# Optimization experiments

Hardware: AMD Instinct MI355X
Metric: run time of the kernel (lower is better)

## Reference

```python
import jax, jax.numpy as jnp
import numpy as np

B, S, H, D = 8, 1024, 8, 64      # batch, seq_len, num_heads, num_hidden
DM = H * D                        # input model dim = 512
DK = 64.0                         # d_k scale
EPS = 1e-3                        # keras GroupNormalization default epsilon


def setup_inputs() -> dict:
    key = jax.random.key(0)
    ks = jax.random.split(key, 12)
    sc = 1.0 / np.sqrt(DM)
    return {
        "query":  jax.random.normal(ks[0], (B, S, DM), jnp.float32),
        "key":    jax.random.normal(ks[1], (B, S, DM), jnp.float32),
        "values": jax.random.normal(ks[2], (B, S, DM), jnp.float32),
        "Wq": jax.random.normal(ks[3], (DM, 3 * H * D), jnp.float32) * sc,
        "bq": jnp.zeros((3 * H * D,), jnp.float32),
        "Wk": jax.random.normal(ks[4], (DM, 2 * H * D), jnp.float32) * sc,
        "bk": jnp.zeros((2 * H * D,), jnp.float32),
        "Wv": jax.random.normal(ks[5], (DM, H * D), jnp.float32) * sc,
        "bv": jnp.zeros((H * D,), jnp.float32),
        "gamma": jnp.ones((D,), jnp.float32),
        "beta": jnp.zeros((D,), jnp.float32),
        "lam": jax.random.uniform(ks[6], (1,), jnp.float32),          # trainable lambda
        "lambda_init": jax.random.uniform(ks[7], (1,), jnp.float32),  # frozen lambda_init
    }


def reference(query, key, values, Wq, bq, Wk, bk, Wv, bv, gamma, beta, lam, lambda_init):
    # projections -> (B, H, S, *)
    q = (query @ Wq + bq).reshape(B, S, H, 3 * D).transpose(0, 2, 1, 3)
    k = (key @ Wk + bk).reshape(B, S, H, 2 * D).transpose(0, 2, 1, 3)
    v = (values @ Wv + bv).reshape(B, S, H, D).transpose(0, 2, 1, 3)

    q1, q2, gate = jnp.split(q, 3, axis=-1)      # each (B,H,S,D)
    k1, k2 = k[..., :D], k[..., D:]

    inv = 1.0 / jnp.sqrt(jnp.float32(DK))
    s1 = jnp.einsum("bhqd,bhkd->bhqk", q1, k1) * inv
    s2 = jnp.einsum("bhqd,bhkd->bhqk", q2, k2) * inv

    # differential attention: dual softmax combined with learned lambda
    attn = jax.nn.softmax(s1, axis=-1) - lam[0] * jax.nn.softmax(s2, axis=-1)
    out = jnp.einsum("bhqk,bhkd->bhqd", attn, v)      # (B,H,S,D)
    out = out.transpose(0, 2, 1, 3)                    # (B,S,H,D)

    # keras GroupNormalization(groups=H, axis=-1) on channels D:
    # reshape channel dim into (groups, D//H), reduce over all non-batch,
    # non-group axes: (S, H, D//H)
    g = out.reshape(B, S, H, H, D // H)
    mean = jnp.mean(g, axis=(1, 2, 4), keepdims=True)
    var = jnp.var(g, axis=(1, 2, 4), keepdims=True)
    g = (g - mean) * jax.lax.rsqrt(var + EPS)
    out = g.reshape(B, S, H, D) * gamma + beta

    out = out * (1.0 - lambda_init[0])
    out = out * jax.nn.sigmoid(gate.transpose(0, 2, 1, 3))
    return out.reshape(B, S, H * D)
```

## Files before the change

### kernel.cpp

```cpp
#include <hip/hip_runtime.h>
#include <cstdint>
#include <cstddef>

#define B_ 8
#define S_ 1024
#define H_ 8
#define D_ 64
#define DM_ 512

typedef __bf16 bf16x8 __attribute__((ext_vector_type(8)));
typedef float floatx4 __attribute__((ext_vector_type(4)));
typedef unsigned short ushort8 __attribute__((ext_vector_type(8)));
typedef unsigned short ushort4v __attribute__((ext_vector_type(4)));

union Frag { ushort8 us; bf16x8 bf; };
union FragU { uint32_t u[4]; bf16x8 bf; };

#define MFMA(a, b, c) __builtin_amdgcn_mfma_f32_16x16x32_bf16((a), (b), (c), 0, 0, 0)

__device__ __forceinline__ unsigned short f2bf(float f) {
  unsigned int u = __float_as_uint(f);
  unsigned int r = (u + 0x7fffu + ((u >> 16) & 1u)) >> 16;
  return (unsigned short)r;
}

__device__ __forceinline__ void gload16(const void* g, void* l) {
  __builtin_amdgcn_global_load_lds(
      (const __attribute__((address_space(1))) unsigned int*)g,
      (__attribute__((address_space(3))) unsigned int*)l, 16, 0, 0);
}

__global__ __launch_bounds__(256) void prep_kernel(
    const float* __restrict__ q, const float* __restrict__ k,
    const float* __restrict__ v, unsigned short* __restrict__ abf,
    const float* __restrict__ Wq, const float* __restrict__ Wk,
    const float* __restrict__ Wv, unsigned short* __restrict__ wt)
{
  __shared__ unsigned short sT[64][72];
  const int tid = threadIdx.x;
  if (blockIdx.x < 12288) {
    size_t i4 = ((size_t)blockIdx.x * 256 + tid) * 4;
    const size_t SEG = (size_t)4 << 20;
    const float* src = (i4 < SEG) ? (q + i4)
                     : (i4 < 2 * SEG) ? (k + (i4 - SEG))
                                      : (v + (i4 - 2 * SEG));
    floatx4 f = *(const floatx4*)src;
    ushort4v o;
    o[0] = f2bf(f[0]); o[1] = f2bf(f[1]); o[2] = f2bf(f[2]); o[3] = f2bf(f[3]);
    *(ushort4v*)(abf + i4) = o;
    return;
  }
  const int bid = blockIdx.x - 12288;
  const int k0 = (bid & 7) * 64;
  const int n0 = (bid >> 3) * 64;
  const float* src; int ncols, nb;
  if (n0 < 1536)      { src = Wq; ncols = 1536; nb = n0; }
  else if (n0 < 2560) { src = Wk; ncols = 1024; nb = n0 - 1536; }
  else                { src = Wv; ncols = 512;  nb = n0 - 2560; }

  const int kr0 = tid >> 4, nc4 = (tid & 15) * 4;
  #pragma unroll
  for (int i = 0; i < 4; i++) {
    int kr = kr0 + i * 16;
    floatx4 f = *(const floatx4*)(src + (size_t)(k0 + kr) * ncols + nb + nc4);
    sT[nc4 + 0][kr] = f2bf(f[0]);
    sT[nc4 + 1][kr] = f2bf(f[1]);
    sT[nc4 + 2][kr] = f2bf(f[2]);
    sT[nc4 + 3][kr] = f2bf(f[3]);
  }
  __syncthreads();
  const int nr0 = tid >> 3, kc8 = (tid & 7) * 8;
  #pragma unroll
  for (int i = 0; i < 2; i++) {
    int nr = nr0 + i * 32;
    *(ushort8*)(wt + (size_t)(n0 + nr) * 512 + k0 + kc8) = *(const ushort8*)&sT[nr][kc8];
  }
}

__global__ __launch_bounds__(256) void gemm_kernel(
    const unsigned short* __restrict__ abf, const unsigned short* __restrict__ wt,
    const float* __restrict__ bq, const float* __restrict__ bk,
    const float* __restrict__ bv,
    unsigned short* __restrict__ q1, unsigned short* __restrict__ q2,
    float* __restrict__ gate, unsigned short* __restrict__ k1,
    unsigned short* __restrict__ k2, unsigned short* __restrict__ vT)
{
  const int tid  = threadIdx.x;
  const int wave = tid >> 6;
  const int lane = tid & 63;
  const int l16  = lane & 15;
  const int quad = lane >> 4;
  const int mt = blockIdx.x;
  const int nt = blockIdx.y;
  const int wm = wave & 1, wn = wave >> 1;

  const unsigned short* Asrc =
      abf + (nt < 12 ? 0 : nt < 20 ? ((size_t)4 << 20) : ((size_t)8 << 20));

  __shared__ unsigned short sMem[2 * 128 * 64];
  unsigned short* sA = sMem;
  unsigned short* sB = sMem + 128 * 64;

  floatx4 acc[4][4];
  #pragma unroll
  for (int i = 0; i < 4; i++)
    #pragma unroll
    for (int j = 0; j < 4; j++)
      #pragma unroll
      for (int r = 0; r < 4; r++) acc[i][j][r] = 0.0f;

  const int lrow   = lane >> 3;
  const int lchunk = lane & 7;
  const int gchunk = lchunk ^ lrow;
  const int rkey   = l16 & 7;

  for (int kt = 0; kt < 8; kt++) {
    #pragma unroll
    for (int j = 0; j < 4; j++) {
      int r8 = (wave * 4 + j) * 8;
      gload16(Asrc + (size_t)(mt * 128 + r8 + lrow) * 512 + kt * 64 + gchunk * 8,
              &sA[(wave * 4 + j) * 512]);
      gload16(wt + (size_t)(nt * 128 + r8 + lrow) * 512 + kt * 64 + gchunk * 8,
              &sB[(wave * 4 + j) * 512]);
    }
    __syncthreads();
    #pragma unroll
    for (int c = 0; c < 2; c++) {
      Frag af[4], bf[4];
      #pragma unroll
      for (int mi = 0; mi < 4; mi++)
        af[mi].us = *(const ushort8*)&sA[(wm * 64 + mi * 16 + l16) * 64 +
                                         (((c * 4 + quad) ^ rkey) << 3)];
      #pragma unroll
      for (int ni = 0; ni < 4; ni++)
        bf[ni].us = *(const ushort8*)&sB[(wn * 64 + ni * 16 + l16) * 64 +
                                         (((c * 4 + quad) ^ rkey) << 3)];
      #pragma unroll
      for (int mi = 0; mi < 4; mi++)
        #pragma unroll
        for (int ni = 0; ni < 4; ni++)
          acc[mi][ni] = MFMA(af[mi].bf, bf[ni].bf, acc[mi][ni]);
    }
    __syncthreads();
  }

  const int gm0 = mt * 128 + wm * 64;
  const int bb  = gm0 >> 10;
  const int s0  = gm0 & 1023;
  const int nseg = nt * 2 + wn;
  unsigned short* sC = sMem + wave * 4096;

  int h, sel = 0; bool isV = false;
  const float* bias_arr; int nb0;
  unsigned short* dstb = nullptr;
  if (nseg < 24)      { h = nseg / 3; sel = nseg % 3; bias_arr = bq; nb0 = nseg * 64;
                        dstb = (sel == 0) ? q1 : (sel == 1) ? q2 : nullptr; }
  else if (nseg < 40) { int t = nseg - 24; h = t >> 1; sel = t & 1;
                        bias_arr = bk; nb0 = t * 64; dstb = sel ? k2 : k1; }
  else                { h = nseg - 40; isV = true; bias_arr = bv; nb0 = (nseg - 40) * 64; }

  if (dstb != nullptr || isV) {
    #pragma unroll
    for (int ni = 0; ni < 4; ni++) {
      float bv_ = bias_arr[nb0 + ni * 16 + l16];
      #pragma unroll
      for (int mi = 0; mi < 4; mi++)
        #pragma unroll
        for (int r = 0; r < 4; r++) {
          float val = acc[mi][ni][r] + bv_;
          int ml = mi * 16 + quad * 4 + r;
          int nl = ni * 16 + l16;
          if (!isV) {
            int ch = (nl >> 3) ^ (ml & 7);
            sC[ml * 64 + (ch << 3) + (nl & 7)] = f2bf(val);
          } else {
            int ch = (ml >> 3) ^ (nl & 7);
            sC[nl * 64 + (ch << 3) + (ml & 7)] = f2bf(val);
          }
        }
    }
    const int rr = lane >> 3, cc = lane & 7;
    if (!isV) {
      unsigned short* base = dstb + ((size_t)(bb * H_ + h) * S_ + s0) * D_;
      #pragma unroll
      for (int j = 0; j < 8; j++) {
        int row = j * 8 + rr;
        int logc = cc ^ (row & 7);
        ushort8 valv = *(const ushort8*)&sC[row * 64 + cc * 8];
        *(ushort8*)(base + (size_t)row * D_ + logc * 8) = valv;
      }
    } else {
      unsigned short* base = vT + ((size_t)(bb * H_ + h) * D_) * S_ + s0;
      #pragma unroll
      for (int j = 0; j < 8; j++) {
        int drow = j * 8 + rr;
        int logc = cc ^ (drow & 7);
        ushort8 valv = *(const ushort8*)&sC[drow * 64 + cc * 8];
        *(ushort8*)(base + (size_t)drow * S_ + logc * 8) = valv;
      }
    }
  } else {
    #pragma unroll
    for (int ni = 0; ni < 4; ni++) {
      float bv_ = bias_arr[nb0 + ni * 16 + l16];
      #pragma unroll
      for (int mi = 0; mi < 4; mi++)
        #pragma unroll
        for (int r = 0; r < 4; r++) {
          int s = s0 + mi * 16 + quad * 4 + r;
          int d = ni * 16 + l16;
          gate[((size_t)(bb * H_ + h) * S_ + s) * D_ + d] = acc[mi][ni][r] + bv_;
        }
    }
  }
}

__global__ __launch_bounds__(256, 4) void attn_kernel(
    const unsigned short* __restrict__ q1, const unsigned short* __restrict__ q2,
    const unsigned short* __restrict__ k1, const unsigned short* __restrict__ k2,
    const unsigned short* __restrict__ vT, const float* __restrict__ lamp,
    float* __restrict__ O)
{
  const int tid  = threadIdx.x;
  const int wave = tid >> 6;
  const int lane = tid & 63;
  const int l16  = lane & 15;
  const int quad = lane >> 4;
  const int bh = blockIdx.x & 63;
  const int qt = blockIdx.x >> 6;

  __shared__ unsigned short sMem[3 * 4096];
  unsigned short* sK1 = sMem;
  unsigned short* sK2 = sMem + 4096;
  unsigned short* sVt = sMem + 8192;

  const int q0 = qt * 64;
  const size_t qoff = ((size_t)bh * S_ + q0 + wave * 16 + l16) * D_;
  Frag qf1[2], qf2[2];
  #pragma unroll
  for (int c = 0; c < 2; c++) {
    qf1[c].us = *(const ushort8*)(q1 + qoff + c * 32 + quad * 8);
    qf2[c].us = *(const ushort8*)(q2 + qoff + c * 32 + quad * 8);
  }

  floatx4 o1t[4], o2t[4];
  float l1 = 0.f, l2 = 0.f;
  #pragma unroll
  for (int i = 0; i < 4; i++)
    #pragma unroll
    for (int j = 0; j < 4; j++) { o1t[i][j] = 0.f; o2t[i][j] = 0.f; }

  const unsigned short* kb1 = k1 + (size_t)bh * S_ * D_;
  const unsigned short* kb2 = k2 + (size_t)bh * S_ * D_;
  const unsigned short* vb  = vT + (size_t)bh * D_ * S_;

  const int srow = lane >> 3;
  const int sgch = (lane & 7) ^ srow;
  const int rkey = l16 & 7;

  for (int kt = 0; kt < 16; kt++) {
    #pragma unroll
    for (int i = 0; i < 2; i++) {
      int r0 = wave * 16 + i * 8;
      gload16(kb1 + (size_t)(kt * 64 + r0 + srow) * 64 + sgch * 8, &sK1[r0 * 64]);
      gload16(kb2 + (size_t)(kt * 64 + r0 + srow) * 64 + sgch * 8, &sK2[r0 * 64]);
      gload16(vb  + (size_t)(r0 + srow) * S_ + kt * 64 + sgch * 8, &sVt[r0 * 64]);
    }
    __syncthreads();

    floatx4 s1[4], s2[4];
    #pragma unroll
    for (int nt = 0; nt < 4; nt++)
      #pragma unroll
      for (int j = 0; j < 4; j++) { s1[nt][j] = 0.f; s2[nt][j] = 0.f; }
    #pragma unroll
    for (int c = 0; c < 2; c++)
      #pragma unroll
      for (int nt = 0; nt < 4; nt++) {
        Frag kf1; kf1.us = *(const ushort8*)&sK1[(nt * 16 + l16) * 64 +
                                                 (((c * 4 + quad) ^ rkey) << 3)];
        s1[nt] = MFMA(kf1.bf, qf1[c].bf, s1[nt]);
        Frag kf2; kf2.us = *(const ushort8*)&sK2[(nt * 16 + l16) * 64 +
                                                 (((c * 4 + quad) ^ rkey) << 3)];
        s2[nt] = MFMA(kf2.bf, qf2[c].bf, s2[nt]);
      }

    uint32_t pk1[4][2], pk2[4][2];
    #pragma unroll
    for (int nt = 0; nt < 4; nt++)
      #pragma unroll
      for (int h = 0; h < 2; h++) {
        float a1 = __expf(s1[nt][2 * h]     * 0.125f);
        float b1v = __expf(s1[nt][2 * h + 1] * 0.125f);
        l1 += a1 + b1v;
        pk1[nt][h] = (uint32_t)f2bf(a1) | ((uint32_t)f2bf(b1v) << 16);
        float a2 = __expf(s2[nt][2 * h]     * 0.125f);
        float b2v = __expf(s2[nt][2 * h + 1] * 0.125f);
        l2 += a2 + b2v;
        pk2[nt][h] = (uint32_t)f2bf(a2) | ((uint32_t)f2bf(b2v) << 16);
      }

    #pragma unroll
    for (int c = 0; c < 2; c++) {
      FragU b1, b2;
      #pragma unroll
      for (int p = 0; p < 4; p++) {
        int src = l16 + ((((quad << 1) + (p >> 1)) & 3) << 4);
        int h = p & 1;
        int lo1 = __shfl((int)pk1[c * 2][h],     src, 64);
        int hi1 = __shfl((int)pk1[c * 2 + 1][h], src, 64);
        b1.u[p] = (quad & 2) ? (uint32_t)hi1 : (uint32_t)lo1;
        int lo2 = __shfl((int)pk2[c * 2][h],     src, 64);
        int hi2 = __shfl((int)pk2[c * 2 + 1][h], src, 64);
        b2.u[p] = (quad & 2) ? (uint32_t)hi2 : (uint32_t)lo2;
      }
      #pragma unroll
      for (int dt = 0; dt < 4; dt++) {
        Frag vf; vf.us = *(const ushort8*)&sVt[(dt * 16 + l16) * 64 +
                                               (((c * 4 + quad) ^ rkey) << 3)];
        o1t[dt] = MFMA(vf.bf, b1.bf, o1t[dt]);
        o2t[dt] = MFMA(vf.bf, b2.bf, o2t[dt]);
      }
    }
    __syncthreads();
  }

  l1 += __shfl_xor(l1, 16, 64); l1 += __shfl_xor(l1, 32, 64);
  l2 += __shfl_xor(l2, 16, 64); l2 += __shfl_xor(l2, 32, 64);

  const float lam = lamp[0];
  const float i1 = 1.0f / l1;
  const float i2 = lam / l2;

  float* fO = (float*)sMem;
  #pragma unroll
  for (int dt = 0; dt < 4; dt++)
    #pragma unroll
    for (int r = 0; r < 4; r++) {
      int d = dt * 16 + quad * 4 + r;
      fO[d * 65 + wave * 16 + l16] = o1t[dt][r] * i1 - o2t[dt][r] * i2;
    }
  __syncthreads();

  float* Ob = O + ((size_t)bh * S_ + q0) * D_;
  #pragma unroll
  for (int i = 0; i < 4; i++) {
    int qrow = i * 16 + (tid >> 4);
    int d0 = (tid & 15) * 4;
    floatx4 v;
    #pragma unroll
    for (int j = 0; j < 4; j++) v[j] = fO[(d0 + j) * 65 + qrow];
    *(floatx4*)(Ob + (size_t)qrow * D_ + d0) = v;
  }
}

__global__ __launch_bounds__(256) void stats1(const float* __restrict__ O,
                                              float* __restrict__ partial)
{
  const int g = blockIdx.x >> 2, ch = blockIdx.x & 3;
  const int b = g >> 3, j = g & 7;
  const float* base = O + (size_t)b * 8 * 65536;
  float s = 0.f, s2 = 0.f;
  for (int t = threadIdx.x; t < 16384; t += 256) {
    int hh = t >> 11;
    int ss = ch * 256 + ((t >> 3) & 255);
    int r  = t & 7;
    float x = base[(size_t)hh * 65536 + ss * 64 + j * 8 + r];
    s += x; s2 += x * x;
  }
  #pragma unroll
  for (int m = 32; m; m >>= 1) { s += __shfl_down(s, m); s2 += __shfl_down(s2, m); }
  __shared__ float red[8];
  if ((threadIdx.x & 63) == 0) {
    red[(threadIdx.x >> 6) * 2]     = s;
    red[(threadIdx.x >> 6) * 2 + 1] = s2;
  }
  __syncthreads();
  if (threadIdx.x == 0) {
    float S1 = 0.f, S2 = 0.f;
    #pragma unroll
    for (int w = 0; w < 4; w++) { S1 += red[w * 2]; S2 += red[w * 2 + 1]; }
    partial[blockIdx.x * 2]     = S1;
    partial[blockIdx.x * 2 + 1] = S2;
  }
}

__global__ __launch_bounds__(256) void final_kernel(
    const float* __restrict__ O, const float* __restrict__ gate,
    const float* __restrict__ partial, const float* __restrict__ gamma,
    const float* __restrict__ beta, const float* __restrict__ li,
    float* __restrict__ out)
{
  int e = blockIdx.x * 256 + threadIdx.x;
  int d  = e & 63;
  int hh = (e >> 6) & 7;
  int s  = (e >> 9) & 1023;
  int b  = e >> 19;
  size_t oidx = (size_t)(b * 8 + hh) * 65536 + (size_t)s * 64 + d;
  int g = b * 8 + (d >> 3);
  float S1 = 0.f, S2 = 0.f;
  #pragma unroll
  for (int ch = 0; ch < 4; ch++) {
    S1 += partial[(g * 4 + ch) * 2];
    S2 += partial[(g * 4 + ch) * 2 + 1];
  }
  float mean = S1 * (1.0f / 65536.f);
  float inv  = rsqrtf(S2 * (1.0f / 65536.f) - mean * mean + 0.001f);
  float x = (O[oidx] - mean) * inv;
  x = x * gamma[d] + beta[d];
  x *= (1.0f - li[0]);
  float gt = gate[oidx];
  x *= 1.0f / (1.0f + __expf(-gt));
  out[e] = x;
}

extern "C" void kernel_launch(void* const* d_in, const int* in_sizes, int n_in,
                              void* d_out, int out_size, void* d_ws, size_t ws_size,
                              hipStream_t stream)
{
  const float* query  = (const float*)d_in[0];
  const float* key    = (const float*)d_in[1];
  const float* values = (const float*)d_in[2];
  const float* Wq = (const float*)d_in[3];
  const float* bq = (const float*)d_in[4];
  const float* Wk = (const float*)d_in[5];
  const float* bk = (const float*)d_in[6];
  const float* Wv = (const float*)d_in[7];
  const float* bv = (const float*)d_in[8];
  const float* gamma = (const float*)d_in[9];
  const float* beta  = (const float*)d_in[10];
  const float* lam   = (const float*)d_in[11];
  const float* lami  = (const float*)d_in[12];
  float* out = (float*)d_out;

  char* ws = (char*)d_ws;
  const size_t MB = (size_t)1 << 20;
  unsigned short* abf = (unsigned short*)(ws);
  float*          O   = (float*)(ws);
  unsigned short* wt  = (unsigned short*)(ws + 24 * MB);
  float* partial      = (float*)(ws + 27 * MB);
  unsigned short* q1  = (unsigned short*)(ws + 28 * MB);
  unsigned short* q2  = (unsigned short*)(ws + 36 * MB);
  unsigned short* k1  = (unsigned short*)(ws + 44 * MB);
  unsigned short* k2  = (unsigned short*)(ws + 52 * MB);
  unsigned short* vT  = (unsigned short*)(ws + 60 * MB);
  float* gate         = (float*)(ws + 68 * MB);

  prep_kernel<<<12672, 256, 0, stream>>>(query, key, values, abf, Wq, Wk, Wv, wt);
  gemm_kernel<<<dim3(64, 24), 256, 0, stream>>>(abf, wt, bq, bk, bv,
                                                q1, q2, gate, k1, k2, vT);
  attn_kernel<<<dim3(1024), 256, 0, stream>>>(q1, q2, k1, k2, vT, lam, O);
  stats1<<<256, 256, 0, stream>>>(O, partial);
  final_kernel<<<16384, 256, 0, stream>>>(O, gate, partial, gamma, beta, lami, out);
}
```

Baseline: 253.1 us.

## Use 32x32 MFMA in attention, stage P via LDS, fuse group-norm stats

The attention kernel moves from 16x16x32 to 32x32x16 bf16 MFMA tiles, with waves split across query and key halves. Softmax probabilities now go through a swizzled LDS buffer instead of cross-lane shuffles, and the 1/sqrt(dk) scale is folded into the q projection epilogue. The separate group-norm stats kernel is removed: attention blocks accumulate sums and sums of squares into a zeroed partial buffer via shared and global atomics, and the prep kernel gains an extra block to zero that buffer. This trades extra LDS traffic, barriers and atomics for fewer shuffles, one fewer launch and no second pass over O.

Measured after the change: 242.9 us. 1.04x faster.

```diff
diff --git a/kernel.cpp b/kernel.cpp
--- a/kernel.cpp
+++ b/kernel.cpp
@@ -10,13 +10,14 @@
 
 typedef __bf16 bf16x8 __attribute__((ext_vector_type(8)));
 typedef float floatx4 __attribute__((ext_vector_type(4)));
+typedef float floatx16 __attribute__((ext_vector_type(16)));
 typedef unsigned short ushort8 __attribute__((ext_vector_type(8)));
 typedef unsigned short ushort4v __attribute__((ext_vector_type(4)));
 
 union Frag { ushort8 us; bf16x8 bf; };
-union FragU { uint32_t u[4]; bf16x8 bf; };
-
-#define MFMA(a, b, c) __builtin_amdgcn_mfma_f32_16x16x32_bf16((a), (b), (c), 0, 0, 0)
+
+#define MFMA16(a, b, c) __builtin_amdgcn_mfma_f32_16x16x32_bf16((a), (b), (c), 0, 0, 0)
+#define MFMA32(a, b, c) __builtin_amdgcn_mfma_f32_32x32x16_bf16((a), (b), (c), 0, 0, 0)
 
 __device__ __forceinline__ unsigned short f2bf(float f) {
   unsigned int u = __float_as_uint(f);
@@ -34,7 +35,8 @@
     const float* __restrict__ q, const float* __restrict__ k,
     const float* __restrict__ v, unsigned short* __restrict__ abf,
     const float* __restrict__ Wq, const float* __restrict__ Wk,
-    const float* __restrict__ Wv, unsigned short* __restrict__ wt)
+    const float* __restrict__ Wv, unsigned short* __restrict__ wt,
+    float* __restrict__ partial)
 {
   __shared__ unsigned short sT[64][72];
   const int tid = threadIdx.x;
@@ -48,6 +50,10 @@
     ushort4v o;
     o[0] = f2bf(f[0]); o[1] = f2bf(f[1]); o[2] = f2bf(f[2]); o[3] = f2bf(f[3]);
     *(ushort4v*)(abf + i4) = o;
+    return;
+  }
+  if (blockIdx.x == 12672) {
+    if (tid < 128) partial[tid] = 0.f;
     return;
   }
   const int bid = blockIdx.x - 12288;
@@ -110,8 +116,7 @@
       for (int r = 0; r < 4; r++) acc[i][j][r] = 0.0f;
 
   const int lrow   = lane >> 3;
-  const int lchunk = lane & 7;
-  const int gchunk = lchunk ^ lrow;
+  const int gchunk = (lane & 7) ^ lrow;
   const int rkey   = l16 & 7;
 
   for (int kt = 0; kt < 8; kt++) {
@@ -139,7 +144,7 @@
       for (int mi = 0; mi < 4; mi++)
         #pragma unroll
         for (int ni = 0; ni < 4; ni++)
-          acc[mi][ni] = MFMA(af[mi].bf, bf[ni].bf, acc[mi][ni]);
+          acc[mi][ni] = MFMA16(af[mi].bf, bf[ni].bf, acc[mi][ni]);
     }
     __syncthreads();
   }
@@ -160,6 +165,7 @@
   else                { h = nseg - 40; isV = true; bias_arr = bv; nb0 = (nseg - 40) * 64; }
 
   if (dstb != nullptr || isV) {
+    const float scl = (nseg < 24) ? 0.125f : 1.0f;
     #pragma unroll
     for (int ni = 0; ni < 4; ni++) {
       float bv_ = bias_arr[nb0 + ni * 16 + l16];
@@ -167,7 +173,7 @@
       for (int mi = 0; mi < 4; mi++)
         #pragma unroll
         for (int r = 0; r < 4; r++) {
-          float val = acc[mi][ni][r] + bv_;
+          float val = (acc[mi][ni][r] + bv_) * scl;
           int ml = mi * 16 + quad * 4 + r;
           int nl = ni * 16 + l16;
           if (!isV) {
@@ -219,36 +225,38 @@
     const unsigned short* __restrict__ q1, const unsigned short* __restrict__ q2,
     const unsigned short* __restrict__ k1, const unsigned short* __restrict__ k2,
     const unsigned short* __restrict__ vT, const float* __restrict__ lamp,
-    float* __restrict__ O)
+    float* __restrict__ O, float* __restrict__ partial)
 {
-  const int tid  = threadIdx.x;
-  const int wave = tid >> 6;
-  const int lane = tid & 63;
-  const int l16  = lane & 15;
-  const int quad = lane >> 4;
+  const int tid   = threadIdx.x;
+  const int wave  = tid >> 6;
+  const int lane  = tid & 63;
+  const int l32   = lane & 31;
+  const int lhalf = lane >> 5;
+  const int kh    = wave & 1;
+  const int qh    = wave >> 1;
   const int bh = blockIdx.x & 63;
   const int qt = blockIdx.x >> 6;
-
-  __shared__ unsigned short sMem[3 * 4096];
+  const int q0 = qt * 64;
+
+  __shared__ unsigned short sMem[5 * 4096];
   unsigned short* sK1 = sMem;
   unsigned short* sK2 = sMem + 4096;
   unsigned short* sVt = sMem + 8192;
-
-  const int q0 = qt * 64;
-  const size_t qoff = ((size_t)bh * S_ + q0 + wave * 16 + l16) * D_;
-  Frag qf1[2], qf2[2];
-  #pragma unroll
-  for (int c = 0; c < 2; c++) {
-    qf1[c].us = *(const ushort8*)(q1 + qoff + c * 32 + quad * 8);
-    qf2[c].us = *(const ushort8*)(q2 + qoff + c * 32 + quad * 8);
-  }
-
-  floatx4 o1t[4], o2t[4];
+  unsigned short* sP1 = sMem + 12288;
+  unsigned short* sP2 = sMem + 16384;
+
+  const size_t qrowoff = ((size_t)bh * S_ + q0 + qh * 32 + l32) * D_ + lhalf * 8;
+  Frag qb1[4], qb2[4];
+  #pragma unroll
+  for (int ks = 0; ks < 4; ks++) {
+    qb1[ks].us = *(const ushort8*)(q1 + qrowoff + ks * 16);
+    qb2[ks].us = *(const ushort8*)(q2 + qrowoff + ks * 16);
+  }
+
+  floatx16 o1, o2;
+  #pragma unroll
+  for (int r = 0; r < 16; r++) { o1[r] = 0.f; o2[r] = 0.f; }
   float l1 = 0.f, l2 = 0.f;
-  #pragma unroll
-  for (int i = 0; i < 4; i++)
-    #pragma unroll
-    for (int j = 0; j < 4; j++) { o1t[i][j] = 0.f; o2t[i][j] = 0.f; }
 
   const unsigned short* kb1 = k1 + (size_t)bh * S_ * D_;
   const unsigned short* kb2 = k2 + (size_t)bh * S_ * D_;
@@ -256,7 +264,8 @@
 
   const int srow = lane >> 3;
   const int sgch = (lane & 7) ^ srow;
-  const int rkey = l16 & 7;
+  const int akey = l32 & 7;
+  const int mrow = kh * 32 + l32;
 
   for (int kt = 0; kt < 16; kt++) {
     #pragma unroll
@@ -268,121 +277,89 @@
     }
     __syncthreads();
 
-    floatx4 s1[4], s2[4];
-    #pragma unroll
-    for (int nt = 0; nt < 4; nt++)
-      #pragma unroll
-      for (int j = 0; j < 4; j++) { s1[nt][j] = 0.f; s2[nt][j] = 0.f; }
-    #pragma unroll
-    for (int c = 0; c < 2; c++)
-      #pragma unroll
-      for (int nt = 0; nt < 4; nt++) {
-        Frag kf1; kf1.us = *(const ushort8*)&sK1[(nt * 16 + l16) * 64 +
-                                                 (((c * 4 + quad) ^ rkey) << 3)];
-        s1[nt] = MFMA(kf1.bf, qf1[c].bf, s1[nt]);
-        Frag kf2; kf2.us = *(const ushort8*)&sK2[(nt * 16 + l16) * 64 +
-                                                 (((c * 4 + quad) ^ rkey) << 3)];
-        s2[nt] = MFMA(kf2.bf, qf2[c].bf, s2[nt]);
-      }
-
-    uint32_t pk1[4][2], pk2[4][2];
-    #pragma unroll
-    for (int nt = 0; nt < 4; nt++)
-      #pragma unroll
-      for (int h = 0; h < 2; h++) {
-        float a1 = __expf(s1[nt][2 * h]     * 0.125f);
-        float b1v = __expf(s1[nt][2 * h + 1] * 0.125f);
-        l1 += a1 + b1v;
-        pk1[nt][h] = (uint32_t)f2bf(a1) | ((uint32_t)f2bf(b1v) << 16);
-        float a2 = __expf(s2[nt][2 * h]     * 0.125f);
-        float b2v = __expf(s2[nt][2 * h + 1] * 0.125f);
-        l2 += a2 + b2v;
-        pk2[nt][h] = (uint32_t)f2bf(a2) | ((uint32_t)f2bf(b2v) << 16);
-      }
-
-    #pragma unroll
-    for (int c = 0; c < 2; c++) {
-      FragU b1, b2;
-      #pragma unroll
-      for (int p = 0; p < 4; p++) {
-        int src = l16 + ((((quad << 1) + (p >> 1)) & 3) << 4);
-        int h = p & 1;
-        int lo1 = __shfl((int)pk1[c * 2][h],     src, 64);
-        int hi1 = __shfl((int)pk1[c * 2 + 1][h], src, 64);
-        b1.u[p] = (quad & 2) ? (uint32_t)hi1 : (uint32_t)lo1;
-        int lo2 = __shfl((int)pk2[c * 2][h],     src, 64);
-        int hi2 = __shfl((int)pk2[c * 2 + 1][h], src, 64);
-        b2.u[p] = (quad & 2) ? (uint32_t)hi2 : (uint32_t)lo2;
-      }
-      #pragma unroll
-      for (int dt = 0; dt < 4; dt++) {
-        Frag vf; vf.us = *(const ushort8*)&sVt[(dt * 16 + l16) * 64 +
-                                               (((c * 4 + quad) ^ rkey) << 3)];
-        o1t[dt] = MFMA(vf.bf, b1.bf, o1t[dt]);
-        o2t[dt] = MFMA(vf.bf, b2.bf, o2t[dt]);
-      }
+    floatx16 s1, s2;
+    #pragma unroll
+    for (int r = 0; r < 16; r++) { s1[r] = 0.f; s2[r] = 0.f; }
+    #pragma unroll
+    for (int ks = 0; ks < 4; ks++) {
+      int phys = ((ks * 2 + lhalf) ^ akey) << 3;
+      Frag kf1; kf1.us = *(const ushort8*)&sK1[mrow * 64 + phys];
+      s1 = MFMA32(kf1.bf, qb1[ks].bf, s1);
+      Frag kf2; kf2.us = *(const ushort8*)&sK2[mrow * 64 + phys];
+      s2 = MFMA32(kf2.bf, qb2[ks].bf, s2);
+    }
+
+    const int qrow = (qh * 32 + l32) * 64;
+    #pragma unroll
+    for (int p = 0; p < 8; p++) {
+      int key = kh * 32 + 2 * (p & 1) + 8 * (p >> 1) + 4 * lhalf;
+      int addr = qrow + (((key >> 3) ^ akey) << 3) + (key & 7);
+      float a1 = __expf(s1[2 * p]), b1 = __expf(s1[2 * p + 1]);
+      l1 += a1 + b1;
+      *(uint32_t*)&sP1[addr] = (uint32_t)f2bf(a1) | ((uint32_t)f2bf(b1) << 16);
+      float a2 = __expf(s2[2 * p]), b2 = __expf(s2[2 * p + 1]);
+      l2 += a2 + b2;
+      *(uint32_t*)&sP2[addr] = (uint32_t)f2bf(a2) | ((uint32_t)f2bf(b2) << 16);
     }
     __syncthreads();
-  }
-
-  l1 += __shfl_xor(l1, 16, 64); l1 += __shfl_xor(l1, 32, 64);
-  l2 += __shfl_xor(l2, 16, 64); l2 += __shfl_xor(l2, 32, 64);
-
-  const float lam = lamp[0];
-  const float i1 = 1.0f / l1;
-  const float i2 = lam / l2;
-
+
+    #pragma unroll
+    for (int ks = 0; ks < 4; ks++) {
+      int phys = ((ks * 2 + lhalf) ^ akey) << 3;
+      Frag vf; vf.us = *(const ushort8*)&sVt[mrow * 64 + phys];
+      Frag pf1; pf1.us = *(const ushort8*)&sP1[qrow + phys];
+      o1 = MFMA32(vf.bf, pf1.bf, o1);
+      Frag pf2; pf2.us = *(const ushort8*)&sP2[qrow + phys];
+      o2 = MFMA32(vf.bf, pf2.bf, o2);
+    }
+    __syncthreads();
+  }
+
+  l1 += __shfl_xor(l1, 32, 64);
+  l2 += __shfl_xor(l2, 32, 64);
+  float* sL = (float*)(sMem + 10240);
+  float* sG = (float*)(sMem + 10752);
+  if (lane < 32) {
+    sL[(0 * 2 + kh) * 64 + qh * 32 + l32] = l1;
+    sL[(1 * 2 + kh) * 64 + qh * 32 + l32] = l2;
+  }
+  __syncthreads();
+
+  const int q = qh * 32 + l32;
+  float i1 = 1.0f / (sL[q] + sL[64 + q]);
+  float i2 = lamp[0] / (sL[128 + q] + sL[192 + q]);
   float* fO = (float*)sMem;
   #pragma unroll
-  for (int dt = 0; dt < 4; dt++)
-    #pragma unroll
-    for (int r = 0; r < 4; r++) {
-      int d = dt * 16 + quad * 4 + r;
-      fO[d * 65 + wave * 16 + l16] = o1t[dt][r] * i1 - o2t[dt][r] * i2;
-    }
+  for (int r = 0; r < 16; r++) {
+    int d = kh * 32 + (r & 3) + 8 * (r >> 2) + 4 * lhalf;
+    fO[d * 65 + q] = o1[r] * i1 - o2[r] * i2;
+  }
+  if (tid < 16) sG[tid] = 0.f;
   __syncthreads();
 
+  float ss = 0.f, ss2 = 0.f;
   float* Ob = O + ((size_t)bh * S_ + q0) * D_;
   #pragma unroll
   for (int i = 0; i < 4; i++) {
-    int qrow = i * 16 + (tid >> 4);
+    int qrw = i * 16 + (tid >> 4);
     int d0 = (tid & 15) * 4;
     floatx4 v;
     #pragma unroll
-    for (int j = 0; j < 4; j++) v[j] = fO[(d0 + j) * 65 + qrow];
-    *(floatx4*)(Ob + (size_t)qrow * D_ + d0) = v;
-  }
-}
-
-__global__ __launch_bounds__(256) void stats1(const float* __restrict__ O,
-                                              float* __restrict__ partial)
-{
-  const int g = blockIdx.x >> 2, ch = blockIdx.x & 3;
-  const int b = g >> 3, j = g & 7;
-  const float* base = O + (size_t)b * 8 * 65536;
-  float s = 0.f, s2 = 0.f;
-  for (int t = threadIdx.x; t < 16384; t += 256) {
-    int hh = t >> 11;
-    int ss = ch * 256 + ((t >> 3) & 255);
-    int r  = t & 7;
-    float x = base[(size_t)hh * 65536 + ss * 64 + j * 8 + r];
-    s += x; s2 += x * x;
-  }
-  #pragma unroll
-  for (int m = 32; m; m >>= 1) { s += __shfl_down(s, m); s2 += __shfl_down(s2, m); }
-  __shared__ float red[8];
-  if ((threadIdx.x & 63) == 0) {
-    red[(threadIdx.x >> 6) * 2]     = s;
-    red[(threadIdx.x >> 6) * 2 + 1] = s2;
+    for (int j = 0; j < 4; j++) {
+      v[j] = fO[(d0 + j) * 65 + qrw];
+      ss += v[j]; ss2 += v[j] * v[j];
+    }
+    *(floatx4*)(Ob + (size_t)qrw * D_ + d0) = v;
+  }
+  ss  += __shfl_xor(ss, 16, 64);  ss  += __shfl_xor(ss, 32, 64);  ss  += __shfl_xor(ss, 1, 64);
+  ss2 += __shfl_xor(ss2, 16, 64); ss2 += __shfl_xor(ss2, 32, 64); ss2 += __shfl_xor(ss2, 1, 64);
+  if (lane < 16 && (lane & 1) == 0) {
+    int j = lane >> 1;
+    atomicAdd(&sG[j * 2],     ss);
+    atomicAdd(&sG[j * 2 + 1], ss2);
   }
   __syncthreads();
-  if (threadIdx.x == 0) {
-    float S1 = 0.f, S2 = 0.f;
-    #pragma unroll
-    for (int w = 0; w < 4; w++) { S1 += red[w * 2]; S2 += red[w * 2 + 1]; }
-    partial[blockIdx.x * 2]     = S1;
-    partial[blockIdx.x * 2 + 1] = S2;
-  }
+  if (tid < 16) atomicAdd(&partial[(bh >> 3) * 16 + tid], sG[tid]);
 }
 
 __global__ __launch_bounds__(256) void final_kernel(
@@ -398,12 +375,8 @@
   int b  = e >> 19;
   size_t oidx = (size_t)(b * 8 + hh) * 65536 + (size_t)s * 64 + d;
   int g = b * 8 + (d >> 3);
-  float S1 = 0.f, S2 = 0.f;
-  #pragma unroll
-  for (int ch = 0; ch < 4; ch++) {
-    S1 += partial[(g * 4 + ch) * 2];
-    S2 += partial[(g * 4 + ch) * 2 + 1];
-  }
+  float S1 = partial[g * 2];
+  float S2 = partial[g * 2 + 1];
   float mean = S1 * (1.0f / 65536.f);
   float inv  = rsqrtf(S2 * (1.0f / 65536.f) - mean * mean + 0.001f);
   float x = (O[oidx] - mean) * inv;
@@ -446,10 +419,10 @@
   unsigned short* vT  = (unsigned short*)(ws + 60 * MB);
   float* gate         = (float*)(ws + 68 * MB);
 
-  prep_kernel<<<12672, 256, 0, stream>>>(query, key, values, abf, Wq, Wk, Wv, wt);
+  prep_kernel<<<12673, 256, 0, stream>>>(query, key, values, abf, Wq, Wk, Wv, wt,
+                                         partial);
   gemm_kernel<<<dim3(64, 24), 256, 0, stream>>>(abf, wt, bq, bk, bv,
                                                 q1, q2, gate, k1, k2, vT);
-  attn_kernel<<<dim3(1024), 256, 0, stream>>>(q1, q2, k1, k2, vT, lam, O);
-  stats1<<<256, 256, 0, stream>>>(O, partial);
+  attn_kernel<<<dim3(1024), 256, 0, stream>>>(q1, q2, k1, k2, vT, lam, O, partial);
   final_kernel<<<16384, 256, 0, stream>>>(O, gate, partial, gamma, beta, lami, out);
 }
```
